# Optimization experiments

Hardware: AMD Instinct MI355X
Metric: run time of the kernel (lower is better)

Reference implementation:

```python
import math
import jax, jax.numpy as jnp
import numpy as np

HIDDEN = 1024
HEADS = 16
HEAD_DIM = HIDDEN // HEADS
PRIME = 7
MAX_ITERS = 10
ENT_THRESH = 0.2
PRIME_SCALE = 1.0 / math.sqrt(PRIME * HEAD_DIM)
EPS = 1e-6


def setup_inputs() -> dict:
    key = jax.random.key(0)
    ks = jax.random.split(key, 6)
    B, S = 2, 2048
    w = 0.02
    return {
        "hidden_states": jax.random.normal(ks[0], (B, S, HIDDEN), jnp.float32),
        "q_w": jax.random.normal(ks[1], (HIDDEN, HIDDEN), jnp.float32) * w,
        "q_b": jnp.zeros((HIDDEN,), jnp.float32),
        "k_w": jax.random.normal(ks[2], (HIDDEN, HIDDEN), jnp.float32) * w,
        "k_b": jnp.zeros((HIDDEN,), jnp.float32),
        "v_w": jax.random.normal(ks[3], (HIDDEN, HIDDEN), jnp.float32) * w,
        "v_b": jnp.zeros((HIDDEN,), jnp.float32),
        "o_w": jax.random.normal(ks[4], (HIDDEN, HIDDEN), jnp.float32) * w,
        "o_b": jnp.zeros((HIDDEN,), jnp.float32),
        "attention_mask": jnp.ones((B, S), jnp.int32),
    }


def _split_heads(x):
    B, S, _ = x.shape
    return x.reshape(B, S, HEADS, HEAD_DIM).transpose(0, 2, 1, 3)


def reference(hidden_states, q_w, q_b, k_w, k_b, v_w, v_b, o_w, o_b, attention_mask):
    B, S, _ = hidden_states.shape
    # projections (torch Linear: x @ W^T + b)
    q = _split_heads(hidden_states @ q_w.T + q_b) * PRIME_SCALE  # [B,H,S,hd]
    k = _split_heads(hidden_states @ k_w.T + k_b)
    v = _split_heads(hidden_states @ v_w.T + v_b)

    scores = jnp.einsum("bhqd,bhkd->bhqk", q, k)  # [B,H,S,S]
    mask = attention_mask[:, None, None, :]
    scores = jnp.where(mask == 0, -jnp.inf, scores)
    attn = jax.nn.softmax(scores, axis=-1)  # dropout p=0 (eval)

    base = jnp.einsum("bhqk,bhkd->bhqd", attn, v)  # attention_weights @ v

    # entropy of the (fixed) attention weights: [B,H]
    entropy = -jnp.sum(attn * jnp.log(attn + EPS), axis=-1).mean(axis=-1)
    avg_entropy = entropy.mean()

    # loop never changes attn, so entropy is constant: either break at i=1 or run all
    full = base
    for i in range(1, MAX_ITERS):
        blend = 1.0 / (1.0 + math.exp(-i / MAX_ITERS))          # sigmoid(i/max)
        res_scale = 0.5 + 0.5 * blend                            # resonance scale
        full = (1.0 - blend) * full + blend * (res_scale * base)

    out_heads = jnp.where(avg_entropy < ENT_THRESH, base, full)  # [B,H,S,hd]

    merged = out_heads.transpose(0, 2, 1, 3).reshape(B, S, HIDDEN)
    return merged @ o_w.T + o_b
```

## Files before the change

kernel.cpp:

```cpp
#include <hip/hip_runtime.h>
#include <hip/hip_bf16.h>
#include <stdint.h>


#define PRIME_SCALE 0.047245559126654356f
#define LOG2E       1.4426950408889634f
#define LN2         0.6931471805599453f
#define QSCALE      (PRIME_SCALE * LOG2E)
#define BLEND_C     0.85096556f

#if __has_builtin(__builtin_amdgcn_exp2f)
#define EXP2(x) __builtin_amdgcn_exp2f(x)
#else
#define EXP2(x) exp2f(x)
#endif

typedef __attribute__((ext_vector_type(8))) short short8;
typedef __attribute__((ext_vector_type(4))) float f32x4;

__device__ __forceinline__ unsigned short f2bf(float x) {
    union { float f; unsigned int u; } v; v.f = x;
    unsigned int r = (v.u + 0x7fffu + ((v.u >> 16) & 1u)) >> 16;
    return (unsigned short)r;
}
__device__ __forceinline__ unsigned short f2bf_fast(float x) {
    union { float f; unsigned int u; } v; v.f = x;
    return (unsigned short)((v.u + 0x8000u) >> 16);
}

__device__ __forceinline__ void glds16(const unsigned short* g, unsigned short* l) {
    __builtin_amdgcn_global_load_lds((const __attribute__((address_space(1))) unsigned int*)g,
                                     (__attribute__((address_space(3))) unsigned int*)l,
                                     16, 0, 0);
}

__global__ void zero_ent(float* p) { p[0] = 0.f; }

__global__ void zero_out_f32(float* p, int n) {
    int i = blockIdx.x * 256 + threadIdx.x;
    if (i < n) p[i] = 0.f;
}

__global__ __launch_bounds__(256) void cvt5(
    const float* __restrict__ s0, const float* __restrict__ s1, const float* __restrict__ s2,
    const float* __restrict__ s3, const float* __restrict__ s4,
    unsigned short* __restrict__ d0, unsigned short* __restrict__ d1, unsigned short* __restrict__ d2,
    unsigned short* __restrict__ d3, unsigned short* __restrict__ d4, float* entp)
{
    if (blockIdx.x == 0 && threadIdx.x == 0) entp[0] = 0.f;
    unsigned int i = blockIdx.x * 256 + threadIdx.x;
    const float* s; unsigned short* d; unsigned int off;
    if (i < (1u << 20)) { s = s0; d = d0; off = i; }
    else {
        unsigned int j = i - (1u << 20);
        unsigned int sel = j >> 18; off = j & 0x3FFFFu;
        s = sel == 0 ? s1 : sel == 1 ? s2 : sel == 2 ? s3 : s4;
        d = sel == 0 ? d1 : sel == 1 ? d2 : sel == 2 ? d3 : d4;
    }
    float4 v = ((const float4*)s)[off];
    ushort4 p; p.x = f2bf(v.x); p.y = f2bf(v.y); p.z = f2bf(v.z); p.w = f2bf(v.w);
    ((ushort4*)d)[off] = p;
}

__global__ __launch_bounds__(256) void gemm_qkv(
    const unsigned short* __restrict__ hsb,
    const unsigned short* __restrict__ qwb, const unsigned short* __restrict__ kwb,
    const unsigned short* __restrict__ vwb,
    const float* __restrict__ qb, const float* __restrict__ kb, const float* __restrict__ vb,
    unsigned short* __restrict__ Qo, unsigned short* __restrict__ Ko, unsigned short* __restrict__ Vto)
{
    const int bid = blockIdx.x;
    const int op = bid >> 8, local = bid & 255;
    const unsigned short *A, *B; const float* bias; unsigned short* C;
    int m0, n0, ldc, biasRow; float scale;
    if (op == 0)      { A = hsb; B = qwb; bias = qb; C = Qo;  m0 = (local >> 3) * 128; n0 = (local & 7) * 128;  ldc = 1024; biasRow = 0; scale = QSCALE; }
    else if (op == 1) { A = hsb; B = kwb; bias = kb; C = Ko;  m0 = (local >> 3) * 128; n0 = (local & 7) * 128;  ldc = 1024; biasRow = 0; scale = 1.f; }
    else              { A = vwb; B = hsb; bias = vb; C = Vto; m0 = (local >> 5) * 128; n0 = (local & 31) * 128; ldc = 4096; biasRow = 1; scale = 1.f; }

    __shared__ unsigned short As[128 * 32];
    __shared__ unsigned short Bs[128 * 32];
    const int t = threadIdx.x, lane = t & 63, w = t >> 6;
    const int quad = lane >> 4, l15 = lane & 15;
    const int wr = (w >> 1) * 64, wc = (w & 1) * 64;
    const int srow = lane >> 2, scol = (lane & 3) * 8;

    f32x4 acc[4][4];
#pragma unroll
    for (int i = 0; i < 4; ++i)
#pragma unroll
        for (int j = 0; j < 4; ++j) acc[i][j] = (f32x4){0.f, 0.f, 0.f, 0.f};

    for (int kk = 0; kk < 32; ++kk) {
        const int k0 = kk * 32;
#pragma unroll
        for (int j = 0; j < 2; ++j) {
            int row = (w * 2 + j) * 16 + srow;
            glds16(&A[(size_t)(m0 + row) * 1024 + k0 + scol], &As[(w * 2 + j) * 512]);
            glds16(&B[(size_t)(n0 + row) * 1024 + k0 + scol], &Bs[(w * 2 + j) * 512]);
        }
        __syncthreads();
        short8 af[4], bf[4];
#pragma unroll
        for (int mt = 0; mt < 4; ++mt) af[mt] = *(const short8*)&As[(wr + mt * 16 + l15) * 32 + quad * 8];
#pragma unroll
        for (int nt = 0; nt < 4; ++nt) bf[nt] = *(const short8*)&Bs[(wc + nt * 16 + l15) * 32 + quad * 8];
#pragma unroll
        for (int mt = 0; mt < 4; ++mt)
#pragma unroll
            for (int nt = 0; nt < 4; ++nt)
                acc[mt][nt] = __builtin_amdgcn_mfma_f32_16x16x32_bf16(af[mt], bf[nt], acc[mt][nt], 0, 0, 0);
        __syncthreads();
    }
#pragma unroll
    for (int mt = 0; mt < 4; ++mt) {
#pragma unroll
        for (int nt = 0; nt < 4; ++nt) {
            int n = n0 + wc + nt * 16 + l15;
#pragma unroll
            for (int r = 0; r < 4; ++r) {
                int m = m0 + wr + mt * 16 + quad * 4 + r;
                float bval = biasRow ? bias[m] : bias[n];
                C[(size_t)m * ldc + n] = f2bf((acc[mt][nt][r] + bval) * scale);
            }
        }
    }
}

__global__ __launch_bounds__(256, 3) void flash_attn(
    const unsigned short* __restrict__ Q,
    const unsigned short* __restrict__ K,
    const unsigned short* __restrict__ Vt,
    const int* __restrict__ mask,
    unsigned short* __restrict__ O,
    float* __restrict__ entp)
{
    const int qt = blockIdx.x;
    const int bh = blockIdx.y;
    const int b = bh >> 4, h = bh & 15;
    const int t = threadIdx.x, lane = t & 63, w = t >> 6;
    const int quad = lane >> 4, l15 = lane & 15;
    const int r8 = lane >> 3, ch8 = lane & 7;

    __shared__ unsigned short Qs[128 * 72];
    __shared__ unsigned short Ks[2][64 * 64];
    __shared__ unsigned short Vs[2][64 * 64];
    __shared__ unsigned int maskBits[64];

    const int* maskb = mask + b * 2048;
    {
        const int4* mp = (const int4*)(maskb + t * 8);
        int4 a = mp[0], c = mp[1];
        unsigned bits = (unsigned)(a.x != 0)       | ((unsigned)(a.y != 0) << 1)
                      | ((unsigned)(a.z != 0) << 2) | ((unsigned)(a.w != 0) << 3)
                      | ((unsigned)(c.x != 0) << 4) | ((unsigned)(c.y != 0) << 5)
                      | ((unsigned)(c.z != 0) << 6) | ((unsigned)(c.w != 0) << 7);
        ((unsigned char*)maskBits)[t] = (unsigned char)bits;
    }
    {
        const int row0 = w * 16;
#pragma unroll
        for (int i = 0; i < 2; ++i) {
            int row = row0 + i * 8 + r8;
            int c = ch8 ^ (row & 7);
            glds16(&K[(size_t)(b * 2048 + row) * 1024 + h * 64 + c * 8], &Ks[0][(row0 + i * 8) * 64]);
            glds16(&Vt[(size_t)(h * 64 + row) * 4096 + b * 2048 + c * 8], &Vs[0][(row0 + i * 8) * 64]);
        }
    }
#pragma unroll
    for (int i = 0; i < 4; ++i) {
        int f = i * 256 + t; int row = f >> 3, c = f & 7;
        uint4 v = *(const uint4*)&Q[(size_t)(b * 2048 + qt * 128 + row) * 1024 + h * 64 + c * 8];
        *(uint4*)&Qs[row * 72 + c * 8] = v;
    }
    __syncthreads();

    short8 qa[2][2];
#pragma unroll
    for (int st = 0; st < 2; ++st) {
        int qrow = w * 32 + st * 16 + l15;
        qa[st][0] = *(const short8*)&Qs[qrow * 72 + quad * 8];
        qa[st][1] = *(const short8*)&Qs[qrow * 72 + 32 + quad * 8];
    }
    unsigned short* Ps = Qs;

    float l_r[2][4], T_r[2][4];
    f32x4 o_acc[2][4];
#pragma unroll
    for (int st = 0; st < 2; ++st)
#pragma unroll
        for (int r = 0; r < 4; ++r) { l_r[st][r] = 0.f; T_r[st][r] = 0.f; }
#pragma unroll
    for (int st = 0; st < 2; ++st)
#pragma unroll
        for (int nt = 0; nt < 4; ++nt) o_acc[st][nt] = (f32x4){0.f, 0.f, 0.f, 0.f};

    for (int kt = 0; kt < 32; ++kt) {
        const int cur = kt & 1;
        if (kt < 31) {
            const int kn = (kt + 1) * 64;
            const int row0 = w * 16;
#pragma unroll
            for (int i = 0; i < 2; ++i) {
                int row = row0 + i * 8 + r8;
                int c = ch8 ^ (row & 7);
                glds16(&K[(size_t)(b * 2048 + kn + row) * 1024 + h * 64 + c * 8], &Ks[cur ^ 1][(row0 + i * 8) * 64]);
                glds16(&Vt[(size_t)(h * 64 + row) * 4096 + b * 2048 + kn + c * 8], &Vs[cur ^ 1][(row0 + i * 8) * 64]);
            }
        }

        f32x4 sacc[2][4];
#pragma unroll
        for (int st = 0; st < 2; ++st)
#pragma unroll
            for (int nt = 0; nt < 4; ++nt) sacc[st][nt] = (f32x4){0.f, 0.f, 0.f, 0.f};
#pragma unroll
        for (int nt = 0; nt < 4; ++nt) {
            int krow = nt * 16 + l15;
            short8 kf0 = *(const short8*)&Ks[cur][krow * 64 + ((quad ^ (krow & 7)) * 8)];
            short8 kf1 = *(const short8*)&Ks[cur][krow * 64 + (((quad + 4) ^ (krow & 7)) * 8)];
#pragma unroll
            for (int st = 0; st < 2; ++st) {
                sacc[st][nt] = __builtin_amdgcn_mfma_f32_16x16x32_bf16(qa[st][0], kf0, sacc[st][nt], 0, 0, 0);
                sacc[st][nt] = __builtin_amdgcn_mfma_f32_16x16x32_bf16(qa[st][1], kf1, sacc[st][nt], 0, 0, 0);
            }
        }
        unsigned mw0 = maskBits[kt * 2], mw1 = maskBits[kt * 2 + 1];
        int mk[4];
        mk[0] = (mw0 >> l15) & 1;
        mk[1] = (mw0 >> (16 + l15)) & 1;
        mk[2] = (mw1 >> l15) & 1;
        mk[3] = (mw1 >> (16 + l15)) & 1;

#pragma unroll
        for (int st = 0; st < 2; ++st) {
#pragma unroll
            for (int r = 0; r < 4; ++r) {
                float s0 = mk[0] ? sacc[st][0][r] : -1.0e30f;
                float s1 = mk[1] ? sacc[st][1][r] : -1.0e30f;
                float s2 = mk[2] ? sacc[st][2][r] : -1.0e30f;
                float s3 = mk[3] ? sacc[st][3][r] : -1.0e30f;
                float p0 = EXP2(s0), p1 = EXP2(s1), p2 = EXP2(s2), p3 = EXP2(s3);
                l_r[st][r] += (p0 + p1) + (p2 + p3);
                T_r[st][r] += (p0 * s0 + p1 * s1) + (p2 * s2 + p3 * s3);
                int pbase = (w * 32 + st * 16 + quad * 4 + r) * 72 + l15;
                Ps[pbase]      = f2bf_fast(p0);
                Ps[pbase + 16] = f2bf_fast(p1);
                Ps[pbase + 32] = f2bf_fast(p2);
                Ps[pbase + 48] = f2bf_fast(p3);
            }
        }

#pragma unroll
        for (int ks = 0; ks < 2; ++ks) {
            short8 pa[2];
#pragma unroll
            for (int st = 0; st < 2; ++st)
                pa[st] = *(const short8*)&Ps[(w * 32 + st * 16 + l15) * 72 + ks * 32 + quad * 8];
#pragma unroll
            for (int nt = 0; nt < 4; ++nt) {
                int vrow = nt * 16 + l15;
                short8 vf = *(const short8*)&Vs[cur][vrow * 64 + ((((ks * 4 + quad)) ^ (vrow & 7)) * 8)];
#pragma unroll
                for (int st = 0; st < 2; ++st)
                    o_acc[st][nt] = __builtin_amdgcn_mfma_f32_16x16x32_bf16(pa[st], vf, o_acc[st][nt], 0, 0, 0);
            }
        }
        __syncthreads();
    }

    float entacc = 0.f;
#pragma unroll
    for (int st = 0; st < 2; ++st) {
#pragma unroll
        for (int r = 0; r < 4; ++r) {
            float l = l_r[st][r], T = T_r[st][r];
            l += __shfl_xor(l, 1); T += __shfl_xor(T, 1);
            l += __shfl_xor(l, 2); T += __shfl_xor(T, 2);
            l += __shfl_xor(l, 4); T += __shfl_xor(T, 4);
            l += __shfl_xor(l, 8); T += __shfl_xor(T, 8);
            float inv = 1.0f / l;
            float ent = LN2 * (__log2f(l) - T * inv);
            if (l15 == 0) entacc += ent;
            int mrow = b * 2048 + qt * 128 + w * 32 + st * 16 + quad * 4 + r;
#pragma unroll
            for (int nt = 0; nt < 4; ++nt)
                O[(size_t)mrow * 1024 + h * 64 + nt * 16 + l15] = f2bf_fast(o_acc[st][nt][r] * inv);
        }
    }
    entacc += __shfl_xor(entacc, 1);
    entacc += __shfl_xor(entacc, 2);
    entacc += __shfl_xor(entacc, 4);
    entacc += __shfl_xor(entacc, 8);
    entacc += __shfl_xor(entacc, 16);
    entacc += __shfl_xor(entacc, 32);
    if (lane == 0) atomicAdd(entp, entacc);
}

__global__ __launch_bounds__(256) void gemm_out_bf(
    const unsigned short* __restrict__ A, const unsigned short* __restrict__ Bw,
    const float* __restrict__ bias, const float* __restrict__ entp,
    float* __restrict__ C)
{
    const float avg = entp[0] * (1.0f / 65536.0f);
    const float scale = (avg < 0.2f) ? 1.0f : BLEND_C;

    const int m0 = blockIdx.x * 128;
    const int n0 = blockIdx.y * 64;
    __shared__ unsigned short As[128 * 32];
    __shared__ unsigned short Bs[64 * 32];
    const int t = threadIdx.x, lane = t & 63, w = t >> 6;
    const int quad = lane >> 4, l15 = lane & 15;
    const int wr = (w >> 1) * 64, wc = (w & 1) * 32;
    const int srow = lane >> 2, scol = (lane & 3) * 8;

    f32x4 acc[4][2];
#pragma unroll
    for (int i = 0; i < 4; ++i)
#pragma unroll
        for (int j = 0; j < 2; ++j) acc[i][j] = (f32x4){0.f, 0.f, 0.f, 0.f};

    for (int kk = 0; kk < 32; ++kk) {
        const int k0 = kk * 32;
#pragma unroll
        for (int j = 0; j < 2; ++j) {
            int row = (w * 2 + j) * 16 + srow;
            glds16(&A[(size_t)(m0 + row) * 1024 + k0 + scol], &As[(w * 2 + j) * 512]);
        }
        {
            int row = w * 16 + srow;
            glds16(&Bw[(size_t)(n0 + row) * 1024 + k0 + scol], &Bs[w * 512]);
        }
        __syncthreads();
        short8 af[4], bf[2];
#pragma unroll
        for (int mt = 0; mt < 4; ++mt) af[mt] = *(const short8*)&As[(wr + mt * 16 + l15) * 32 + quad * 8];
#pragma unroll
        for (int nt = 0; nt < 2; ++nt) bf[nt] = *(const short8*)&Bs[(wc + nt * 16 + l15) * 32 + quad * 8];
#pragma unroll
        for (int mt = 0; mt < 4; ++mt)
#pragma unroll
            for (int nt = 0; nt < 2; ++nt)
                acc[mt][nt] = __builtin_amdgcn_mfma_f32_16x16x32_bf16(af[mt], bf[nt], acc[mt][nt], 0, 0, 0);
        __syncthreads();
    }
#pragma unroll
    for (int mt = 0; mt < 4; ++mt) {
#pragma unroll
        for (int nt = 0; nt < 2; ++nt) {
            int n = n0 + wc + nt * 16 + l15;
#pragma unroll
            for (int r = 0; r < 4; ++r) {
                int m = m0 + wr + mt * 16 + quad * 4 + r;
                C[(size_t)m * 1024 + n] = scale * acc[mt][nt][r] + bias[n];
            }
        }
    }
}

__global__ __launch_bounds__(256) void gemm_nt_f32(
    const float* __restrict__ A, const float* __restrict__ B,
    const float* __restrict__ bias, int biasRow, float scale,
    unsigned short* __restrict__ C, int N)
{
    const int m0 = blockIdx.x * 128;
    const int n0 = blockIdx.y * 128;
    __shared__ unsigned short As[128 * 40];
    __shared__ unsigned short Bs[128 * 40];
    const int t = threadIdx.x, lane = t & 63, w = t >> 6;
    const int wr = (w >> 1) * 64, wc = (w & 1) * 64;
    const int quad = lane >> 4, l15 = lane & 15;

    f32x4 acc[4][4];
#pragma unroll
    for (int i = 0; i < 4; ++i)
#pragma unroll
        for (int j = 0; j < 4; ++j) acc[i][j] = (f32x4){0.f, 0.f, 0.f, 0.f};

    for (int kk = 0; kk < 32; ++kk) {
        const int k0 = kk * 32;
#pragma unroll
        for (int i = 0; i < 4; ++i) {
            int f = i * 256 + t;
            int row = f >> 3, ch = f & 7;
            float4 av = *(const float4*)&A[(size_t)(m0 + row) * 1024 + k0 + ch * 4];
            ushort4 ap; ap.x = f2bf(av.x); ap.y = f2bf(av.y); ap.z = f2bf(av.z); ap.w = f2bf(av.w);
            *(ushort4*)&As[row * 40 + ch * 4] = ap;
            float4 bv = *(const float4*)&B[(size_t)(n0 + row) * 1024 + k0 + ch * 4];
            ushort4 bp; bp.x = f2bf(bv.x); bp.y = f2bf(bv.y); bp.z = f2bf(bv.z); bp.w = f2bf(bv.w);
            *(ushort4*)&Bs[row * 40 + ch * 4] = bp;
        }
        __syncthreads();
        short8 af[4], bfr[4];
#pragma unroll
        for (int mt = 0; mt < 4; ++mt) af[mt] = *(const short8*)&As[(wr + mt * 16 + l15) * 40 + quad * 8];
#pragma unroll
        for (int nt = 0; nt < 4; ++nt) bfr[nt] = *(const short8*)&Bs[(wc + nt * 16 + l15) * 40 + quad * 8];
#pragma unroll
        for (int mt = 0; mt < 4; ++mt)
#pragma unroll
            for (int nt = 0; nt < 4; ++nt)
                acc[mt][nt] = __builtin_amdgcn_mfma_f32_16x16x32_bf16(af[mt], bfr[nt], acc[mt][nt], 0, 0, 0);
        __syncthreads();
    }
#pragma unroll
    for (int mt = 0; mt < 4; ++mt) {
#pragma unroll
        for (int nt = 0; nt < 4; ++nt) {
            int n = n0 + wc + nt * 16 + l15;
#pragma unroll
            for (int r = 0; r < 4; ++r) {
                int m = m0 + wr + mt * 16 + quad * 4 + r;
                float bval = biasRow ? bias[m] : bias[n];
                C[(size_t)m * N + n] = f2bf((acc[mt][nt][r] + bval) * scale);
            }
        }
    }
}

__global__ __launch_bounds__(256) void gemm_out_f32B(
    const unsigned short* __restrict__ A, const float* __restrict__ B,
    const float* __restrict__ bias, const float* __restrict__ entp,
    float* __restrict__ C)
{
    const float avg = entp[0] * (1.0f / 65536.0f);
    const float scale = (avg < 0.2f) ? 1.0f : BLEND_C;

    const int m0 = blockIdx.x * 128;
    const int n0 = blockIdx.y * 128;
    __shared__ unsigned short As[128 * 40];
    __shared__ unsigned short Bs[128 * 40];
    const int t = threadIdx.x, lane = t & 63, w = t >> 6;
    const int wr = (w >> 1) * 64, wc = (w & 1) * 64;
    const int quad = lane >> 4, l15 = lane & 15;

    f32x4 acc[4][4];
#pragma unroll
    for (int i = 0; i < 4; ++i)
#pragma unroll
        for (int j = 0; j < 4; ++j) acc[i][j] = (f32x4){0.f, 0.f, 0.f, 0.f};

    for (int kk = 0; kk < 32; ++kk) {
        const int k0 = kk * 32;
#pragma unroll
        for (int i = 0; i < 2; ++i) {
            int f = i * 256 + t;
            int row = f >> 2, ch = f & 3;
            uint4 av = *(const uint4*)&A[(size_t)(m0 + row) * 1024 + k0 + ch * 8];
            *(uint4*)&As[row * 40 + ch * 8] = av;
        }
#pragma unroll
        for (int i = 0; i < 4; ++i) {
            int f = i * 256 + t;
            int row = f >> 3, ch = f & 7;
            float4 bv = *(const float4*)&B[(size_t)(n0 + row) * 1024 + k0 + ch * 4];
            ushort4 bp; bp.x = f2bf(bv.x); bp.y = f2bf(bv.y); bp.z = f2bf(bv.z); bp.w = f2bf(bv.w);
            *(ushort4*)&Bs[row * 40 + ch * 4] = bp;
        }
        __syncthreads();
        short8 af[4], bfr[4];
#pragma unroll
        for (int mt = 0; mt < 4; ++mt) af[mt] = *(const short8*)&As[(wr + mt * 16 + l15) * 40 + quad * 8];
#pragma unroll
        for (int nt = 0; nt < 4; ++nt) bfr[nt] = *(const short8*)&Bs[(wc + nt * 16 + l15) * 40 + quad * 8];
#pragma unroll
        for (int mt = 0; mt < 4; ++mt)
#pragma unroll
            for (int nt = 0; nt < 4; ++nt)
                acc[mt][nt] = __builtin_amdgcn_mfma_f32_16x16x32_bf16(af[mt], bfr[nt], acc[mt][nt], 0, 0, 0);
        __syncthreads();
    }
#pragma unroll
    for (int mt = 0; mt < 4; ++mt) {
#pragma unroll
        for (int nt = 0; nt < 4; ++nt) {
            int n = n0 + wc + nt * 16 + l15;
#pragma unroll
            for (int r = 0; r < 4; ++r) {
                int m = m0 + wr + mt * 16 + quad * 4 + r;
                C[(size_t)m * 1024 + n] = scale * acc[mt][nt][r] + bias[n];
            }
        }
    }
}

extern "C" void kernel_launch(void* const* d_in, const int* in_sizes, int n_in,
                              void* d_out, int out_size, void* d_ws, size_t ws_size,
                              hipStream_t stream)
{
    const float* hs = (const float*)d_in[0];
    const float* qw = (const float*)d_in[1];
    const float* qb = (const float*)d_in[2];
    const float* kw = (const float*)d_in[3];
    const float* kb = (const float*)d_in[4];
    const float* vw = (const float*)d_in[5];
    const float* vb = (const float*)d_in[6];
    const float* ow = (const float*)d_in[7];
    const float* ob = (const float*)d_in[8];
    const int*   mask = (const int*)d_in[9];
    float* out = (float*)d_out;

    const size_t MB = 1024 * 1024;
    char* ws = (char*)d_ws;
    dim3 blk(256);

    if (ws_size >= 40 * MB + 4) {
        unsigned short* hsb = (unsigned short*)(ws);
        unsigned short* Q   = (unsigned short*)(ws + 8 * MB);
        unsigned short* Kp  = (unsigned short*)(ws + 16 * MB);
        unsigned short* Vt  = (unsigned short*)(ws + 24 * MB);
        unsigned short* qwb = (unsigned short*)(ws + 32 * MB);
        unsigned short* kwb = (unsigned short*)(ws + 34 * MB);
        unsigned short* vwb = (unsigned short*)(ws + 36 * MB);
        unsigned short* owb = (unsigned short*)(ws + 38 * MB);
        float* entp         = (float*)(ws + 40 * MB);
        unsigned short* O   = hsb;

        cvt5<<<dim3(8192), blk, 0, stream>>>(hs, qw, kw, vw, ow, hsb, qwb, kwb, vwb, owb, entp);
        gemm_qkv<<<dim3(768), blk, 0, stream>>>(hsb, qwb, kwb, vwb, qb, kb, vb, Q, Kp, Vt);
        flash_attn<<<dim3(16, 32), blk, 0, stream>>>(Q, Kp, Vt, mask, O, entp);
        gemm_out_bf<<<dim3(32, 16), blk, 0, stream>>>(O, owb, ob, entp, out);
    } else if (ws_size >= 32 * MB + 4) {
        unsigned short* Q  = (unsigned short*)(ws);
        unsigned short* Kp = (unsigned short*)(ws + 8 * MB);
        unsigned short* Vt = (unsigned short*)(ws + 16 * MB);
        unsigned short* O  = (unsigned short*)(ws + 24 * MB);
        float* entp        = (float*)(ws + 32 * MB);

        zero_ent<<<dim3(1), dim3(1), 0, stream>>>(entp);
        gemm_nt_f32<<<dim3(32, 8), blk, 0, stream>>>(hs, qw, qb, 0, QSCALE, Q, 1024);
        gemm_nt_f32<<<dim3(32, 8), blk, 0, stream>>>(hs, kw, kb, 0, 1.0f, Kp, 1024);
        gemm_nt_f32<<<dim3(8, 32), blk, 0, stream>>>(vw, hs, vb, 1, 1.0f, Vt, 4096);
        flash_attn<<<dim3(16, 32), blk, 0, stream>>>(Q, Kp, Vt, mask, O, entp);
        gemm_out_f32B<<<dim3(32, 8), blk, 0, stream>>>(O, ow, ob, entp, out);
    } else {
        zero_out_f32<<<dim3((out_size + 255) / 256), blk, 0, stream>>>(out, out_size);
    }
}
```

Measured before the change: 230.3 us.

## Split attention over key halves with a separate combine kernel

```diff
diff --git a/kernel.cpp b/kernel.cpp
--- a/kernel.cpp
+++ b/kernel.cpp
@@ -26,6 +26,10 @@
 __device__ __forceinline__ unsigned short f2bf_fast(float x) {
     union { float f; unsigned int u; } v; v.f = x;
     return (unsigned short)((v.u + 0x8000u) >> 16);
+}
+__device__ __forceinline__ float bf2f(unsigned short x) {
+    union { unsigned int u; float f; } v; v.u = ((unsigned int)x) << 16;
+    return v.f;
 }
 
 __device__ __forceinline__ void glds16(const unsigned short* g, unsigned short* l) {
@@ -126,6 +130,210 @@
     }
 }
 
+__global__ __launch_bounds__(256, 3) void flash_split(
+    const unsigned short* __restrict__ Q,
+    const unsigned short* __restrict__ K,
+    const unsigned short* __restrict__ Vt,
+    const int* __restrict__ mask,
+    unsigned short* __restrict__ O0, unsigned short* __restrict__ O1,
+    float* __restrict__ lpart, float* __restrict__ Tpart)
+{
+    const int qt = blockIdx.x;
+    const int bh = blockIdx.y;
+    const int z  = blockIdx.z;
+    const int b = bh >> 4, h = bh & 15;
+    const int t = threadIdx.x, lane = t & 63, w = t >> 6;
+    const int quad = lane >> 4, l15 = lane & 15;
+    const int r8 = lane >> 3, ch8 = lane & 7;
+    const int kt0 = z * 16, kt1 = kt0 + 16;
+    unsigned short* __restrict__ Opart = z ? O1 : O0;
+
+    __shared__ unsigned short Qs[128 * 72];
+    __shared__ unsigned short Ks[2][64 * 64];
+    __shared__ unsigned short Vs[2][64 * 64];
+    __shared__ unsigned int maskBits[64];
+
+    const int* maskb = mask + b * 2048;
+    {
+        const int4* mp = (const int4*)(maskb + t * 8);
+        int4 a = mp[0], c = mp[1];
+        unsigned bits = (unsigned)(a.x != 0)       | ((unsigned)(a.y != 0) << 1)
+                      | ((unsigned)(a.z != 0) << 2) | ((unsigned)(a.w != 0) << 3)
+                      | ((unsigned)(c.x != 0) << 4) | ((unsigned)(c.y != 0) << 5)
+                      | ((unsigned)(c.z != 0) << 6) | ((unsigned)(c.w != 0) << 7);
+        ((unsigned char*)maskBits)[t] = (unsigned char)bits;
+    }
+    {
+        const int row0 = w * 16;
+#pragma unroll
+        for (int i = 0; i < 2; ++i) {
+            int row = row0 + i * 8 + r8;
+            int c = ch8 ^ (row & 7);
+            glds16(&K[(size_t)(b * 2048 + kt0 * 64 + row) * 1024 + h * 64 + c * 8], &Ks[0][(row0 + i * 8) * 64]);
+            glds16(&Vt[(size_t)(h * 64 + row) * 4096 + b * 2048 + kt0 * 64 + c * 8], &Vs[0][(row0 + i * 8) * 64]);
+        }
+    }
+#pragma unroll
+    for (int i = 0; i < 4; ++i) {
+        int f = i * 256 + t; int row = f >> 3, c = f & 7;
+        uint4 v = *(const uint4*)&Q[(size_t)(b * 2048 + qt * 128 + row) * 1024 + h * 64 + c * 8];
+        *(uint4*)&Qs[row * 72 + c * 8] = v;
+    }
+    __syncthreads();
+
+    short8 qa[2][2];
+#pragma unroll
+    for (int st = 0; st < 2; ++st) {
+        int qrow = w * 32 + st * 16 + l15;
+        qa[st][0] = *(const short8*)&Qs[qrow * 72 + quad * 8];
+        qa[st][1] = *(const short8*)&Qs[qrow * 72 + 32 + quad * 8];
+    }
+    unsigned short* Ps = Qs;
+
+    float l_r[2][4], T_r[2][4];
+    f32x4 o_acc[2][4];
+#pragma unroll
+    for (int st = 0; st < 2; ++st)
+#pragma unroll
+        for (int r = 0; r < 4; ++r) { l_r[st][r] = 0.f; T_r[st][r] = 0.f; }
+#pragma unroll
+    for (int st = 0; st < 2; ++st)
+#pragma unroll
+        for (int nt = 0; nt < 4; ++nt) o_acc[st][nt] = (f32x4){0.f, 0.f, 0.f, 0.f};
+
+    for (int kt = kt0; kt < kt1; ++kt) {
+        const int cur = kt & 1;
+        if (kt < kt1 - 1) {
+            const int kn = (kt + 1) * 64;
+            const int row0 = w * 16;
+#pragma unroll
+            for (int i = 0; i < 2; ++i) {
+                int row = row0 + i * 8 + r8;
+                int c = ch8 ^ (row & 7);
+                glds16(&K[(size_t)(b * 2048 + kn + row) * 1024 + h * 64 + c * 8], &Ks[cur ^ 1][(row0 + i * 8) * 64]);
+                glds16(&Vt[(size_t)(h * 64 + row) * 4096 + b * 2048 + kn + c * 8], &Vs[cur ^ 1][(row0 + i * 8) * 64]);
+            }
+        }
+
+        f32x4 sacc[2][4];
+#pragma unroll
+        for (int st = 0; st < 2; ++st)
+#pragma unroll
+            for (int nt = 0; nt < 4; ++nt) sacc[st][nt] = (f32x4){0.f, 0.f, 0.f, 0.f};
+#pragma unroll
+        for (int nt = 0; nt < 4; ++nt) {
+            int krow = nt * 16 + l15;
+            short8 kf0 = *(const short8*)&Ks[cur][krow * 64 + ((quad ^ (krow & 7)) * 8)];
+            short8 kf1 = *(const short8*)&Ks[cur][krow * 64 + (((quad + 4) ^ (krow & 7)) * 8)];
+#pragma unroll
+            for (int st = 0; st < 2; ++st) {
+                sacc[st][nt] = __builtin_amdgcn_mfma_f32_16x16x32_bf16(qa[st][0], kf0, sacc[st][nt], 0, 0, 0);
+                sacc[st][nt] = __builtin_amdgcn_mfma_f32_16x16x32_bf16(qa[st][1], kf1, sacc[st][nt], 0, 0, 0);
+            }
+        }
+        unsigned mw0 = maskBits[kt * 2], mw1 = maskBits[kt * 2 + 1];
+        int mk[4];
+        mk[0] = (mw0 >> l15) & 1;
+        mk[1] = (mw0 >> (16 + l15)) & 1;
+        mk[2] = (mw1 >> l15) & 1;
+        mk[3] = (mw1 >> (16 + l15)) & 1;
+
+#pragma unroll
+        for (int st = 0; st < 2; ++st) {
+#pragma unroll
+            for (int r = 0; r < 4; ++r) {
+                float s0 = mk[0] ? sacc[st][0][r] : -1.0e30f;
+                float s1 = mk[1] ? sacc[st][1][r] : -1.0e30f;
+                float s2 = mk[2] ? sacc[st][2][r] : -1.0e30f;
+                float s3 = mk[3] ? sacc[st][3][r] : -1.0e30f;
+                float p0 = EXP2(s0), p1 = EXP2(s1), p2 = EXP2(s2), p3 = EXP2(s3);
+                l_r[st][r] += (p0 + p1) + (p2 + p3);
+                T_r[st][r] += (p0 * s0 + p1 * s1) + (p2 * s2 + p3 * s3);
+                int pbase = (w * 32 + st * 16 + quad * 4 + r) * 72 + l15;
+                Ps[pbase]      = f2bf_fast(p0);
+                Ps[pbase + 16] = f2bf_fast(p1);
+                Ps[pbase + 32] = f2bf_fast(p2);
+                Ps[pbase + 48] = f2bf_fast(p3);
+            }
+        }
+
+#pragma unroll
+        for (int ks = 0; ks < 2; ++ks) {
+            short8 pa[2];
+#pragma unroll
+            for (int st = 0; st < 2; ++st)
+                pa[st] = *(const short8*)&Ps[(w * 32 + st * 16 + l15) * 72 + ks * 32 + quad * 8];
+#pragma unroll
+            for (int nt = 0; nt < 4; ++nt) {
+                int vrow = nt * 16 + l15;
+                short8 vf = *(const short8*)&Vs[cur][vrow * 64 + ((((ks * 4 + quad)) ^ (vrow & 7)) * 8)];
+#pragma unroll
+                for (int st = 0; st < 2; ++st)
+                    o_acc[st][nt] = __builtin_amdgcn_mfma_f32_16x16x32_bf16(pa[st], vf, o_acc[st][nt], 0, 0, 0);
+            }
+        }
+        __syncthreads();
+    }
+
+#pragma unroll
+    for (int st = 0; st < 2; ++st) {
+#pragma unroll
+        for (int r = 0; r < 4; ++r) {
+            float l = l_r[st][r], T = T_r[st][r];
+            l += __shfl_xor(l, 1); T += __shfl_xor(T, 1);
+            l += __shfl_xor(l, 2); T += __shfl_xor(T, 2);
+            l += __shfl_xor(l, 4); T += __shfl_xor(T, 4);
+            l += __shfl_xor(l, 8); T += __shfl_xor(T, 8);
+            int qrow = qt * 128 + w * 32 + st * 16 + quad * 4 + r;
+            if (l15 == 0) {
+                int li = z * 65536 + bh * 2048 + qrow;
+                lpart[li] = l; Tpart[li] = T;
+            }
+            int mrow = b * 2048 + qrow;
+#pragma unroll
+            for (int nt = 0; nt < 4; ++nt)
+                Opart[(size_t)mrow * 1024 + h * 64 + nt * 16 + l15] = f2bf_fast(o_acc[st][nt][r]);
+        }
+    }
+}
+
+__global__ __launch_bounds__(256) void combine_split(
+    unsigned short* __restrict__ O0, const unsigned short* __restrict__ O1,
+    const float* __restrict__ lpart, const float* __restrict__ Tpart,
+    float* __restrict__ entp)
+{
+    unsigned idx = blockIdx.x * 256 + threadIdx.x;
+    int mrow = idx >> 8;
+    int c4 = (idx & 255) << 2;
+    int h = c4 >> 6;
+    int b = mrow >> 11, qrow = mrow & 2047;
+    int li = (b * 16 + h) * 2048 + qrow;
+    float l = lpart[li] + lpart[65536 + li];
+    float inv = 1.0f / l;
+
+    ushort4 a = ((const ushort4*)O0)[idx];
+    ushort4 c = ((const ushort4*)O1)[idx];
+    ushort4 o;
+    o.x = f2bf_fast((bf2f(a.x) + bf2f(c.x)) * inv);
+    o.y = f2bf_fast((bf2f(a.y) + bf2f(c.y)) * inv);
+    o.z = f2bf_fast((bf2f(a.z) + bf2f(c.z)) * inv);
+    o.w = f2bf_fast((bf2f(a.w) + bf2f(c.w)) * inv);
+    ((ushort4*)O0)[idx] = o;
+
+    float ent = 0.f;
+    if ((idx & 15) == 0) {
+        float T = Tpart[li] + Tpart[65536 + li];
+        ent = LN2 * (__log2f(l) - T * inv);
+    }
+    ent += __shfl_xor(ent, 1);
+    ent += __shfl_xor(ent, 2);
+    ent += __shfl_xor(ent, 4);
+    ent += __shfl_xor(ent, 8);
+    ent += __shfl_xor(ent, 16);
+    ent += __shfl_xor(ent, 32);
+    if ((threadIdx.x & 63) == 0) atomicAdd(entp, ent);
+}
+
 __global__ __launch_bounds__(256, 3) void flash_attn(
     const unsigned short* __restrict__ Q,
     const unsigned short* __restrict__ K,
@@ -207,7 +415,6 @@
                 glds16(&Vt[(size_t)(h * 64 + row) * 4096 + b * 2048 + kn + c * 8], &Vs[cur ^ 1][(row0 + i * 8) * 64]);
             }
         }
-
         f32x4 sacc[2][4];
 #pragma unroll
         for (int st = 0; st < 2; ++st)
@@ -230,7 +437,6 @@
         mk[1] = (mw0 >> (16 + l15)) & 1;
         mk[2] = (mw1 >> l15) & 1;
         mk[3] = (mw1 >> (16 + l15)) & 1;
-
 #pragma unroll
         for (int st = 0; st < 2; ++st) {
 #pragma unroll
@@ -249,7 +455,6 @@
                 Ps[pbase + 48] = f2bf_fast(p3);
             }
         }
-
 #pragma unroll
         for (int ks = 0; ks < 2; ++ks) {
             short8 pa[2];
@@ -267,7 +472,6 @@
         }
         __syncthreads();
     }
-
     float entacc = 0.f;
 #pragma unroll
     for (int st = 0; st < 2; ++st) {
@@ -347,132 +551,6 @@
     for (int mt = 0; mt < 4; ++mt) {
 #pragma unroll
         for (int nt = 0; nt < 2; ++nt) {
-            int n = n0 + wc + nt * 16 + l15;
-#pragma unroll
-            for (int r = 0; r < 4; ++r) {
-                int m = m0 + wr + mt * 16 + quad * 4 + r;
-                C[(size_t)m * 1024 + n] = scale * acc[mt][nt][r] + bias[n];
-            }
-        }
-    }
-}
-
-__global__ __launch_bounds__(256) void gemm_nt_f32(
-    const float* __restrict__ A, const float* __restrict__ B,
-    const float* __restrict__ bias, int biasRow, float scale,
-    unsigned short* __restrict__ C, int N)
-{
-    const int m0 = blockIdx.x * 128;
-    const int n0 = blockIdx.y * 128;
-    __shared__ unsigned short As[128 * 40];
-    __shared__ unsigned short Bs[128 * 40];
-    const int t = threadIdx.x, lane = t & 63, w = t >> 6;
-    const int wr = (w >> 1) * 64, wc = (w & 1) * 64;
-    const int quad = lane >> 4, l15 = lane & 15;
-
-    f32x4 acc[4][4];
-#pragma unroll
-    for (int i = 0; i < 4; ++i)
-#pragma unroll
-        for (int j = 0; j < 4; ++j) acc[i][j] = (f32x4){0.f, 0.f, 0.f, 0.f};
-
-    for (int kk = 0; kk < 32; ++kk) {
-        const int k0 = kk * 32;
-#pragma unroll
-        for (int i = 0; i < 4; ++i) {
-            int f = i * 256 + t;
-            int row = f >> 3, ch = f & 7;
-            float4 av = *(const float4*)&A[(size_t)(m0 + row) * 1024 + k0 + ch * 4];
-            ushort4 ap; ap.x = f2bf(av.x); ap.y = f2bf(av.y); ap.z = f2bf(av.z); ap.w = f2bf(av.w);
-            *(ushort4*)&As[row * 40 + ch * 4] = ap;
-            float4 bv = *(const float4*)&B[(size_t)(n0 + row) * 1024 + k0 + ch * 4];
-            ushort4 bp; bp.x = f2bf(bv.x); bp.y = f2bf(bv.y); bp.z = f2bf(bv.z); bp.w = f2bf(bv.w);
-            *(ushort4*)&Bs[row * 40 + ch * 4] = bp;
-        }
-        __syncthreads();
-        short8 af[4], bfr[4];
-#pragma unroll
-        for (int mt = 0; mt < 4; ++mt) af[mt] = *(const short8*)&As[(wr + mt * 16 + l15) * 40 + quad * 8];
-#pragma unroll
-        for (int nt = 0; nt < 4; ++nt) bfr[nt] = *(const short8*)&Bs[(wc + nt * 16 + l15) * 40 + quad * 8];
-#pragma unroll
-        for (int mt = 0; mt < 4; ++mt)
-#pragma unroll
-            for (int nt = 0; nt < 4; ++nt)
-                acc[mt][nt] = __builtin_amdgcn_mfma_f32_16x16x32_bf16(af[mt], bfr[nt], acc[mt][nt], 0, 0, 0);
-        __syncthreads();
-    }
-#pragma unroll
-    for (int mt = 0; mt < 4; ++mt) {
-#pragma unroll
-        for (int nt = 0; nt < 4; ++nt) {
-            int n = n0 + wc + nt * 16 + l15;
-#pragma unroll
-            for (int r = 0; r < 4; ++r) {
-                int m = m0 + wr + mt * 16 + quad * 4 + r;
-                float bval = biasRow ? bias[m] : bias[n];
-                C[(size_t)m * N + n] = f2bf((acc[mt][nt][r] + bval) * scale);
-            }
-        }
-    }
-}
-
-__global__ __launch_bounds__(256) void gemm_out_f32B(
-    const unsigned short* __restrict__ A, const float* __restrict__ B,
-    const float* __restrict__ bias, const float* __restrict__ entp,
-    float* __restrict__ C)
-{
-    const float avg = entp[0] * (1.0f / 65536.0f);
-    const float scale = (avg < 0.2f) ? 1.0f : BLEND_C;
-
-    const int m0 = blockIdx.x * 128;
-    const int n0 = blockIdx.y * 128;
-    __shared__ unsigned short As[128 * 40];
-    __shared__ unsigned short Bs[128 * 40];
-    const int t = threadIdx.x, lane = t & 63, w = t >> 6;
-    const int wr = (w >> 1) * 64, wc = (w & 1) * 64;
-    const int quad = lane >> 4, l15 = lane & 15;
-
-    f32x4 acc[4][4];
-#pragma unroll
-    for (int i = 0; i < 4; ++i)
-#pragma unroll
-        for (int j = 0; j < 4; ++j) acc[i][j] = (f32x4){0.f, 0.f, 0.f, 0.f};
-
-    for (int kk = 0; kk < 32; ++kk) {
-        const int k0 = kk * 32;
-#pragma unroll
-        for (int i = 0; i < 2; ++i) {
-            int f = i * 256 + t;
-            int row = f >> 2, ch = f & 3;
-            uint4 av = *(const uint4*)&A[(size_t)(m0 + row) * 1024 + k0 + ch * 8];
-            *(uint4*)&As[row * 40 + ch * 8] = av;
-        }
-#pragma unroll
-        for (int i = 0; i < 4; ++i) {
-            int f = i * 256 + t;
-            int row = f >> 3, ch = f & 7;
-            float4 bv = *(const float4*)&B[(size_t)(n0 + row) * 1024 + k0 + ch * 4];
-            ushort4 bp; bp.x = f2bf(bv.x); bp.y = f2bf(bv.y); bp.z = f2bf(bv.z); bp.w = f2bf(bv.w);
-            *(ushort4*)&Bs[row * 40 + ch * 4] = bp;
-        }
-        __syncthreads();
-        short8 af[4], bfr[4];
-#pragma unroll
-        for (int mt = 0; mt < 4; ++mt) af[mt] = *(const short8*)&As[(wr + mt * 16 + l15) * 40 + quad * 8];
-#pragma unroll
-        for (int nt = 0; nt < 4; ++nt) bfr[nt] = *(const short8*)&Bs[(wc + nt * 16 + l15) * 40 + quad * 8];
-#pragma unroll
-        for (int mt = 0; mt < 4; ++mt)
-#pragma unroll
-            for (int nt = 0; nt < 4; ++nt)
-                acc[mt][nt] = __builtin_amdgcn_mfma_f32_16x16x32_bf16(af[mt], bfr[nt], acc[mt][nt], 0, 0, 0);
-        __syncthreads();
-    }
-#pragma unroll
-    for (int mt = 0; mt < 4; ++mt) {
-#pragma unroll
-        for (int nt = 0; nt < 4; ++nt) {
             int n = n0 + wc + nt * 16 + l15;
 #pragma unroll
             for (int r = 0; r < 4; ++r) {
@@ -503,7 +581,27 @@
     char* ws = (char*)d_ws;
     dim3 blk(256);
 
-    if (ws_size >= 40 * MB + 4) {
+    if (ws_size >= 50 * MB) {
+        unsigned short* hsb = (unsigned short*)(ws);
+        unsigned short* Q   = (unsigned short*)(ws + 8 * MB);
+        unsigned short* Kp  = (unsigned short*)(ws + 16 * MB);
+        unsigned short* Vt  = (unsigned short*)(ws + 24 * MB);
+        unsigned short* qwb = (unsigned short*)(ws + 32 * MB);
+        unsigned short* kwb = (unsigned short*)(ws + 34 * MB);
+        unsigned short* vwb = (unsigned short*)(ws + 36 * MB);
+        unsigned short* owb = (unsigned short*)(ws + 38 * MB);
+        float* entp         = (float*)(ws + 40 * MB);
+        unsigned short* Op1 = (unsigned short*)(ws + 41 * MB);
+        float* lpart        = (float*)(ws + 49 * MB);
+        float* Tpart        = (float*)(ws + 49 * MB + 524288);
+        unsigned short* Op0 = hsb;
+
+        cvt5<<<dim3(8192), blk, 0, stream>>>(hs, qw, kw, vw, ow, hsb, qwb, kwb, vwb, owb, entp);
+        gemm_qkv<<<dim3(768), blk, 0, stream>>>(hsb, qwb, kwb, vwb, qb, kb, vb, Q, Kp, Vt);
+        flash_split<<<dim3(16, 32, 2), blk, 0, stream>>>(Q, Kp, Vt, mask, Op0, Op1, lpart, Tpart);
+        combine_split<<<dim3(4096), blk, 0, stream>>>(Op0, Op1, lpart, Tpart, entp);
+        gemm_out_bf<<<dim3(32, 16), blk, 0, stream>>>(Op0, owb, ob, entp, out);
+    } else if (ws_size >= 40 * MB + 4) {
         unsigned short* hsb = (unsigned short*)(ws);
         unsigned short* Q   = (unsigned short*)(ws + 8 * MB);
         unsigned short* Kp  = (unsigned short*)(ws + 16 * MB);
@@ -519,19 +617,6 @@
         gemm_qkv<<<dim3(768), blk, 0, stream>>>(hsb, qwb, kwb, vwb, qb, kb, vb, Q, Kp, Vt);
         flash_attn<<<dim3(16, 32), blk, 0, stream>>>(Q, Kp, Vt, mask, O, entp);
         gemm_out_bf<<<dim3(32, 16), blk, 0, stream>>>(O, owb, ob, entp, out);
-    } else if (ws_size >= 32 * MB + 4) {
-        unsigned short* Q  = (unsigned short*)(ws);
-        unsigned short* Kp = (unsigned short*)(ws + 8 * MB);
-        unsigned short* Vt = (unsigned short*)(ws + 16 * MB);
-        unsigned short* O  = (unsigned short*)(ws + 24 * MB);
-        float* entp        = (float*)(ws + 32 * MB);
-
-        zero_ent<<<dim3(1), dim3(1), 0, stream>>>(entp);
-        gemm_nt_f32<<<dim3(32, 8), blk, 0, stream>>>(hs, qw, qb, 0, QSCALE, Q, 1024);
-        gemm_nt_f32<<<dim3(32, 8), blk, 0, stream>>>(hs, kw, kb, 0, 1.0f, Kp, 1024);
-        gemm_nt_f32<<<dim3(8, 32), blk, 0, stream>>>(vw, hs, vb, 1, 1.0f, Vt, 4096);
-        flash_attn<<<dim3(16, 32), blk, 0, stream>>>(Q, Kp, Vt, mask, O, entp);
-        gemm_out_f32B<<<dim3(32, 8), blk, 0, stream>>>(O, ow, ob, entp, out);
     } else {
         zero_out_f32<<<dim3((out_size + 255) / 256), blk, 0, stream>>>(out, out_size);
     }
```

New measurement: 419.3 us. 82.0% more time.
